# Optimization experiments

Hardware: AMD Instinct MI355X
Metric: run time of the kernel (lower is better)

The kernel has to match this reference:

```python
import jax, jax.numpy as jnp
import numpy as np

K = 3       # kernel_size
STRIDE = 1
PAD = 1
EPS = 1e-12  # F.normalize eps


def setup_inputs() -> dict:
    key = jax.random.key(0)
    k1, k2, k3 = jax.random.split(key, 3)
    x = jax.random.normal(k1, (8, 128, 112, 112), dtype=jnp.float32)
    weight = jax.random.normal(k2, (256, 128, K, K), dtype=jnp.float32)
    bias = jax.random.normal(k3, (256,), dtype=jnp.float32)
    return {"x": x, "weight": weight, "bias": bias}


def reference(x, weight, bias):
    B, C, H, W = x.shape
    Cout = weight.shape[0]
    oh = (H + 2 * PAD - K) // STRIDE + 1
    ow = (W + 2 * PAD - K) // STRIDE + 1
    # im2col: [B, C*K*K, oh, ow]; feature order (C, kh, kw), same as torch F.unfold
    patches = jax.lax.conv_general_dilated_patches(
        x, (K, K), (STRIDE, STRIDE), [(PAD, PAD), (PAD, PAD)],
        dimension_numbers=("NCHW", "OIHW", "NCHW"))
    u = patches.reshape(B, C * K * K, oh * ow)
    # L2-normalize each patch column (dim=1), matching F.normalize(p=2, dim=1)
    norm = jnp.sqrt(jnp.sum(u * u, axis=1, keepdims=True))
    u = u / jnp.maximum(norm, EPS)
    # GEMM: [Cout, C*K*K] x [B, C*K*K, L] -> [B, Cout, L]
    out = jnp.einsum("od,bdl->bol", weight.reshape(Cout, -1), u)
    out = out.reshape(B, Cout, oh, ow) + bias[None, :, None, None]
    return out
```

## Files before the change

kernel.cpp:

```cpp
#include <hip/hip_runtime.h>

#define CIN    128
#define COUT   256
#define Hh     112
#define Ww     112
#define HW     12544
#define NBATCH 8
#define NPIX   (NBATCH*HW)
#define KD     (CIN*9)
#define PH     114
#define PPIX   (NBATCH*PH*PH)

typedef __bf16         v8bf __attribute__((ext_vector_type(8)));
typedef float          v4f  __attribute__((ext_vector_type(4)));

__device__ __forceinline__ unsigned short f2bf(float f) {
  unsigned int u = __float_as_uint(f);
  u += 0x7FFFu + ((u >> 16) & 1u);
  return (unsigned short)(u >> 16);
}

__device__ __forceinline__ void gl_lds16(const void* g, void* l) {
  __builtin_amdgcn_global_load_lds(
      (const __attribute__((address_space(1))) void*)g,
      (__attribute__((address_space(3))) void*)l, 16, 0, 0);
}

#define SQS 65
__global__ __launch_bounds__(256) void k_sq_convert(
    const float* __restrict__ x, unsigned short* __restrict__ xbp,
    float* __restrict__ sq)
{
  __shared__ unsigned int US[56 * SQS];
  __shared__ float sqp[56 * 4];

  int tid = threadIdx.x;
  int l   = tid & 63;
  int wid = tid >> 6;
  int bid = blockIdx.x;
  int xh  = bid & 1;
  int t2  = bid >> 1;
  int b   = t2 / Hh;
  int oy  = t2 - b * Hh;
  int ox0 = xh * 56;

  const float* xp = x + (size_t)b * CIN * HW + oy * Ww + ox0;
  bool valid = l < 56;
  float acc = 0.0f;
#pragma unroll
  for (int it = 0; it < 16; ++it) {
    int cp = it * 4 + wid;
    int c0 = cp * 2;
    float v0 = 0.0f, v1 = 0.0f;
    if (valid) {
      v0 = xp[(size_t)c0 * HW + l];
      v1 = xp[(size_t)(c0 + 1) * HW + l];
    }
    acc += v0 * v0 + v1 * v1;
    unsigned int pk = (unsigned int)f2bf(v0) | ((unsigned int)f2bf(v1) << 16);
    if (valid) US[l * SQS + cp] = pk;
  }
  if (valid) sqp[l * 4 + wid] = acc;
  __syncthreads();

  if (tid < 56) {
    float s = sqp[tid * 4] + sqp[tid * 4 + 1] + sqp[tid * 4 + 2] + sqp[tid * 4 + 3];
    sq[(size_t)b * HW + oy * Ww + ox0 + tid] = s;
  }

  unsigned int* dst = (unsigned int*)xbp +
      ((size_t)(b * PH + oy + 1) * PH + (ox0 + 1)) * (CIN / 2);
  for (int h = tid; h < 896; h += 256) {
    int u0  = h * 4;
    int pix = u0 >> 6, cu = u0 & 63;
    const unsigned int* s = &US[pix * SQS + cu];
    uint4 vv; vv.x = s[0]; vv.y = s[1]; vv.z = s[2]; vv.w = s[3];
    *(uint4*)(dst + u0) = vv;
  }
}

__global__ __launch_bounds__(256) void k_zero_border(unsigned short* __restrict__ xbp)
{
  int gid = blockIdx.x * 256 + threadIdx.x;
  if (gid >= PPIX) return;
  int b  = gid / (PH * PH);
  int r  = gid - b * PH * PH;
  int py = r / PH;
  int px = r - py * PH;
  if (py != 0 && py != PH - 1 && px != 0 && px != PH - 1) return;
  unsigned int* dst = (unsigned int*)xbp + (size_t)gid * (CIN / 2);
  uint4 z = {0, 0, 0, 0};
#pragma unroll
  for (int c0 = 0; c0 < 64; c0 += 4) *(uint4*)(dst + c0) = z;
}

__global__ __launch_bounds__(256) void k_invnorm(
    const float* __restrict__ sq, float* __restrict__ invn)
{
  int p = blockIdx.x * 256 + threadIdx.x;
  if (p >= NPIX) return;
  int b  = p / HW;  int r  = p - b * HW;
  int oy = r / Ww;  int ox = r - oy * Ww;
  const float* s = sq + (size_t)b * HW;
  float acc = 0.0f;
#pragma unroll
  for (int dy = -1; dy <= 1; ++dy) {
    int iy = oy + dy;
    if (iy < 0 || iy >= Hh) continue;
#pragma unroll
    for (int dx = -1; dx <= 1; ++dx) {
      int ix = ox + dx;
      if (ix < 0 || ix >= Ww) continue;
      acc += s[iy * Ww + ix];
    }
  }
  invn[p] = 1.0f / fmaxf(sqrtf(acc), 1e-12f);
}

__global__ __launch_bounds__(256) void k_packw(
    const float* __restrict__ w, unsigned short* __restrict__ wp)
{
  int idx = blockIdx.x * 256 + threadIdx.x;
  int o  = idx / KD;
  int rr = idx - o * KD;
  int kk = rr >> 7;
  int c  = rr & 127;
  wp[idx] = f2bf(w[(size_t)o * KD + c * 9 + kk]);
}

#define SLAB_S 132
__global__ __launch_bounds__(256, 3) void k_conv(
    const unsigned short* __restrict__ wp,
    const unsigned short* __restrict__ xbp,
    const float* __restrict__ invn,
    const float* __restrict__ bias,
    float* __restrict__ out)
{
  __shared__ __align__(16) char smem[64 * SLAB_S * 4];
  unsigned short* As = (unsigned short*)smem;
  unsigned short* Bs = As + 128 * 64;
  float* slab = (float*)smem;

  int tid  = threadIdx.x;
  int lane = tid & 63;
  int wid  = tid >> 6;
  int wm   = wid >> 1, wn = wid & 1;
  int quad = lane >> 4;
  int l16  = lane & 15;

  int L  = blockIdx.x;
  int g  = L >> 4;
  int j  = L & 15;
  int bn = g * 8 + (j & 7);
  int bm = j >> 3;

  int srow = tid >> 3;
  int g16  = (tid & 7) ^ (srow & 7);

  const unsigned short* asrc = wp + (size_t)(bm * 128 + srow) * KD + g16 * 8;

  int pb[4];
#pragma unroll
  for (int jj = 0; jj < 4; ++jj) {
    int n  = bn * 128 + jj * 32 + srow;
    int b  = n / HW;  int r  = n - b * HW;
    int oy = r / Ww;  int ox = r - oy * Ww;
    pb[jj] = ((b * PH + oy) * PH + ox) * CIN + g16 * 8;
  }

  v4f acc[4][4];
#pragma unroll
  for (int mt = 0; mt < 4; ++mt)
#pragma unroll
    for (int nt = 0; nt < 4; ++nt)
#pragma unroll
      for (int q = 0; q < 4; ++q) acc[mt][nt][q] = 0.0f;

  const int khs[9] = {0,0,0,1,1,1,2,2,2};
  const int kws[9] = {0,1,2,0,1,2,0,1,2};

  for (int s = 0; s < 18; ++s) {
    int kk   = s >> 1;
    int c0   = (s & 1) * 64;
    int soff = (khs[kk] * PH + kws[kk]) * CIN + c0;

#pragma unroll
    for (int jj = 0; jj < 4; ++jj)
      gl_lds16(asrc + (size_t)jj * 32 * KD + s * 64,
               &As[(wid * 8 + jj * 32) * 64]);
#pragma unroll
    for (int jj = 0; jj < 4; ++jj)
      gl_lds16(xbp + pb[jj] + soff,
               &Bs[(wid * 8 + jj * 32) * 64]);

    __syncthreads();

#pragma unroll
    for (int h = 0; h < 2; ++h) {
      v8bf af[4], bf[4];
      int cch = (h * 4 + quad) ^ (l16 & 7);
#pragma unroll
      for (int mt = 0; mt < 4; ++mt)
        af[mt] = *(const v8bf*)&As[(wm * 64 + mt * 16 + l16) * 64 + cch * 8];
#pragma unroll
      for (int nt = 0; nt < 4; ++nt)
        bf[nt] = *(const v8bf*)&Bs[(wn * 64 + nt * 16 + l16) * 64 + cch * 8];
#pragma unroll
      for (int mt = 0; mt < 4; ++mt)
#pragma unroll
        for (int nt = 0; nt < 4; ++nt)
          acc[mt][nt] = __builtin_amdgcn_mfma_f32_16x16x32_bf16(
              af[mt], bf[nt], acc[mt][nt], 0, 0, 0);
    }

    __syncthreads();
  }

  int nbase = bn * 128;
  int bb = nbase / HW;
  int rr = nbase - bb * HW;
  float* obase = out + (size_t)bb * COUT * HW + rr;

  float invv[4];
#pragma unroll
  for (int nt = 0; nt < 4; ++nt)
    invv[nt] = invn[nbase + wn * 64 + nt * 16 + l16];

  for (int pass = 0; pass < 2; ++pass) {
    if (pass) __syncthreads();
    if (wm == pass) {
#pragma unroll
      for (int mt = 0; mt < 4; ++mt)
#pragma unroll
        for (int nt = 0; nt < 4; ++nt) {
          int col = wn * 64 + nt * 16 + l16;
#pragma unroll
          for (int reg = 0; reg < 4; ++reg)
            slab[(mt * 16 + quad * 4 + reg) * SLAB_S + col] =
                acc[mt][nt][reg] * invv[nt];
        }
    }
    __syncthreads();
#pragma unroll
    for (int it = 0; it < 2; ++it) {
      int row = it * 32 + (tid >> 3);
      int o   = bm * 128 + pass * 64 + row;
      float bv = bias[o];
      float* orow = obase + (size_t)o * HW;
#pragma unroll
      for (int k = 0; k < 4; ++k) {
        int c4 = ((tid & 7) + k * 8) * 4;
        v4f v = *(const v4f*)&slab[row * SLAB_S + c4];
        v4f r2;
#pragma unroll
        for (int q = 0; q < 4; ++q) r2[q] = v[q] + bv;
        *(v4f*)(orow + c4) = r2;
      }
    }
  }
}

extern "C" void kernel_launch(void* const* d_in, const int* in_sizes, int n_in,
                              void* d_out, int out_size, void* d_ws, size_t ws_size,
                              hipStream_t stream) {
  const float* x    = (const float*)d_in[0];
  const float* w    = (const float*)d_in[1];
  const float* bias = (const float*)d_in[2];
  float* out        = (float*)d_out;

  char* ws = (char*)d_ws;
  unsigned short* xbp = (unsigned short*)ws;
  size_t off = (size_t)PPIX * CIN * 2;
  unsigned short* wpk = (unsigned short*)(ws + off);
  off += (size_t)COUT * KD * 2;
  float* sq = (float*)(ws + off);
  off += (size_t)NPIX * 4;
  float* invn = (float*)(ws + off);

  k_sq_convert<<<NBATCH * Hh * 2, 256, 0, stream>>>(x, xbp, sq);
  k_zero_border<<<(PPIX + 255) / 256, 256, 0, stream>>>(xbp);
  k_packw<<<(COUT * KD) / 256, 256, 0, stream>>>(w, wpk);
  k_invnorm<<<NPIX / 256, 256, 0, stream>>>(sq, invn);
  k_conv<<<1568, 256, 0, stream>>>(wpk, xbp, invn, bias, out);
}
```

Measured before the change: 216.2 us.

## Merge prep kernels into one launch and fold norm stencil into conv epilogue

The four preprocessing kernels (bf16 conversion with squared sums, border zeroing, weight packing, inverse-norm) collapse into a single k_prep launch. Block-index ranges split that launch into conversion, border-only zeroing and vectorized weight-pack work. The 3x3 inverse-norm stencil now runs in the conv epilogue straight from the squared sums. This removes three launches and one intermediate buffer pass, at the cost of extra scattered loads and a division in each conv block's epilogue.

Measured after the change: 218.2 us. About the same (+0.9%).

```diff
diff --git a/kernel.cpp b/kernel.cpp
--- a/kernel.cpp
+++ b/kernel.cpp
@@ -11,6 +11,10 @@
 #define PH     114
 #define PPIX   (NBATCH*PH*PH)
 
+#define G_SQ   784
+#define G_BORD 226
+#define G_PACK 288
+
 typedef __bf16         v8bf __attribute__((ext_vector_type(8)));
 typedef float          v4f  __attribute__((ext_vector_type(4)));
 
@@ -26,113 +30,93 @@
       (__attribute__((address_space(3))) void*)l, 16, 0, 0);
 }
 
-#define SQS 65
-__global__ __launch_bounds__(256) void k_sq_convert(
-    const float* __restrict__ x, unsigned short* __restrict__ xbp,
-    float* __restrict__ sq)
+#define USS 65
+__global__ __launch_bounds__(256) void k_prep(
+    const float* __restrict__ x, const float* __restrict__ w,
+    unsigned short* __restrict__ xbp, float* __restrict__ sq,
+    unsigned short* __restrict__ wp)
 {
-  __shared__ unsigned int US[56 * SQS];
-  __shared__ float sqp[56 * 4];
-
+  int bid = blockIdx.x;
   int tid = threadIdx.x;
-  int l   = tid & 63;
-  int wid = tid >> 6;
-  int bid = blockIdx.x;
-  int xh  = bid & 1;
-  int t2  = bid >> 1;
-  int b   = t2 / Hh;
-  int oy  = t2 - b * Hh;
-  int ox0 = xh * 56;
-
-  const float* xp = x + (size_t)b * CIN * HW + oy * Ww + ox0;
-  bool valid = l < 56;
-  float acc = 0.0f;
-#pragma unroll
-  for (int it = 0; it < 16; ++it) {
-    int cp = it * 4 + wid;
-    int c0 = cp * 2;
-    float v0 = 0.0f, v1 = 0.0f;
-    if (valid) {
-      v0 = xp[(size_t)c0 * HW + l];
-      v1 = xp[(size_t)(c0 + 1) * HW + l];
-    }
-    acc += v0 * v0 + v1 * v1;
-    unsigned int pk = (unsigned int)f2bf(v0) | ((unsigned int)f2bf(v1) << 16);
-    if (valid) US[l * SQS + cp] = pk;
-  }
-  if (valid) sqp[l * 4 + wid] = acc;
-  __syncthreads();
-
-  if (tid < 56) {
-    float s = sqp[tid * 4] + sqp[tid * 4 + 1] + sqp[tid * 4 + 2] + sqp[tid * 4 + 3];
-    sq[(size_t)b * HW + oy * Ww + ox0 + tid] = s;
-  }
-
-  unsigned int* dst = (unsigned int*)xbp +
-      ((size_t)(b * PH + oy + 1) * PH + (ox0 + 1)) * (CIN / 2);
-  for (int h = tid; h < 896; h += 256) {
-    int u0  = h * 4;
-    int pix = u0 >> 6, cu = u0 & 63;
-    const unsigned int* s = &US[pix * SQS + cu];
-    uint4 vv; vv.x = s[0]; vv.y = s[1]; vv.z = s[2]; vv.w = s[3];
-    *(uint4*)(dst + u0) = vv;
-  }
-}
-
-__global__ __launch_bounds__(256) void k_zero_border(unsigned short* __restrict__ xbp)
-{
-  int gid = blockIdx.x * 256 + threadIdx.x;
-  if (gid >= PPIX) return;
-  int b  = gid / (PH * PH);
-  int r  = gid - b * PH * PH;
-  int py = r / PH;
-  int px = r - py * PH;
-  if (py != 0 && py != PH - 1 && px != 0 && px != PH - 1) return;
-  unsigned int* dst = (unsigned int*)xbp + (size_t)gid * (CIN / 2);
-  uint4 z = {0, 0, 0, 0};
-#pragma unroll
-  for (int c0 = 0; c0 < 64; c0 += 4) *(uint4*)(dst + c0) = z;
-}
-
-__global__ __launch_bounds__(256) void k_invnorm(
-    const float* __restrict__ sq, float* __restrict__ invn)
-{
-  int p = blockIdx.x * 256 + threadIdx.x;
-  if (p >= NPIX) return;
-  int b  = p / HW;  int r  = p - b * HW;
-  int oy = r / Ww;  int ox = r - oy * Ww;
-  const float* s = sq + (size_t)b * HW;
-  float acc = 0.0f;
-#pragma unroll
-  for (int dy = -1; dy <= 1; ++dy) {
-    int iy = oy + dy;
-    if (iy < 0 || iy >= Hh) continue;
-#pragma unroll
-    for (int dx = -1; dx <= 1; ++dx) {
-      int ix = ox + dx;
-      if (ix < 0 || ix >= Ww) continue;
-      acc += s[iy * Ww + ix];
-    }
-  }
-  invn[p] = 1.0f / fmaxf(sqrtf(acc), 1e-12f);
-}
-
-__global__ __launch_bounds__(256) void k_packw(
-    const float* __restrict__ w, unsigned short* __restrict__ wp)
-{
-  int idx = blockIdx.x * 256 + threadIdx.x;
-  int o  = idx / KD;
-  int rr = idx - o * KD;
-  int kk = rr >> 7;
-  int c  = rr & 127;
-  wp[idx] = f2bf(w[(size_t)o * KD + c * 9 + kk]);
+
+  if (bid < G_SQ) {
+    __shared__ unsigned int US[128 * USS];
+    __shared__ float sqp[4 * 128];
+
+    int l   = tid & 63;
+    int wid = tid >> 6;
+    int P0  = bid * 128;
+    int b   = P0 / HW;
+    int r0  = P0 - b * HW;
+
+    const float* xb0 = x + (size_t)b * CIN * HW + r0;
+    float ax = 0.0f, ay = 0.0f;
+#pragma unroll
+    for (int i = 0; i < 16; ++i) {
+      int c = wid * 32 + i * 2;
+      float2 v0 = ((const float2*)(xb0 + (size_t)c * HW))[l];
+      float2 v1 = ((const float2*)(xb0 + (size_t)(c + 1) * HW))[l];
+      ax += v0.x * v0.x + v1.x * v1.x;
+      ay += v0.y * v0.y + v1.y * v1.y;
+      int c2 = wid * 16 + i;
+      US[(2 * l) * USS + c2]     = (unsigned int)f2bf(v0.x) | ((unsigned int)f2bf(v1.x) << 16);
+      US[(2 * l + 1) * USS + c2] = (unsigned int)f2bf(v0.y) | ((unsigned int)f2bf(v1.y) << 16);
+    }
+    sqp[wid * 128 + 2 * l]     = ax;
+    sqp[wid * 128 + 2 * l + 1] = ay;
+    __syncthreads();
+
+    if (tid < 128)
+      sq[P0 + tid] = sqp[tid] + sqp[128 + tid] + sqp[256 + tid] + sqp[384 + tid];
+
+    unsigned int* xout = (unsigned int*)xbp;
+#pragma unroll
+    for (int it = 0; it < 8; ++it) {
+      int h  = it * 256 + tid;
+      int px = h >> 4, cu = (h & 15) * 4;
+      const unsigned int* s = &US[px * USS + cu];
+      uint4 v; v.x = s[0]; v.y = s[1]; v.z = s[2]; v.w = s[3];
+      int p  = P0 + px;
+      int rr = p - b * HW;
+      int oy = rr / Ww, ox = rr - oy * Ww;
+      *(uint4*)(xout + ((size_t)(b * PH + oy + 1) * PH + (ox + 1)) * 64 + cu) = v;
+    }
+    return;
+  }
+
+  if (bid < G_SQ + G_BORD) {
+    int h   = (bid - G_SQ) * 256 + tid;
+    int img = h / (452 * 16);
+    int rem = h - img * (452 * 16);
+    int bp  = rem >> 4;
+    int cu  = (rem & 15) * 4;
+    int y, xq;
+    if      (bp < 114) { y = 0;        xq = bp; }
+    else if (bp < 228) { y = PH - 1;   xq = bp - 114; }
+    else if (bp < 340) { y = bp - 227; xq = 0; }
+    else               { y = bp - 339; xq = PH - 1; }
+    uint4 z = {0, 0, 0, 0};
+    *(uint4*)((unsigned int*)xbp + ((size_t)(img * PH + y) * PH + xq) * 64 + cu) = z;
+    return;
+  }
+
+  int idx = (bid - G_SQ - G_BORD) * 256 + tid;
+  int o   = idx / 288;
+  int rem = idx - o * 288;
+  int kk  = rem >> 5;
+  int c0  = (rem & 31) * 4;
+  const float* ws = w + (size_t)o * KD + kk;
+  unsigned int p0 = (unsigned int)f2bf(ws[(c0 + 0) * 9]) | ((unsigned int)f2bf(ws[(c0 + 1) * 9]) << 16);
+  unsigned int p1 = (unsigned int)f2bf(ws[(c0 + 2) * 9]) | ((unsigned int)f2bf(ws[(c0 + 3) * 9]) << 16);
+  uint2 pk; pk.x = p0; pk.y = p1;
+  *(uint2*)((unsigned int*)wp + ((size_t)o * KD + kk * 128 + c0) / 2) = pk;
 }
 
 #define SLAB_S 132
 __global__ __launch_bounds__(256, 3) void k_conv(
     const unsigned short* __restrict__ wp,
     const unsigned short* __restrict__ xbp,
-    const float* __restrict__ invn,
+    const float* __restrict__ sq,
     const float* __restrict__ bias,
     float* __restrict__ out)
 {
@@ -220,11 +204,28 @@
   int bb = nbase / HW;
   int rr = nbase - bb * HW;
   float* obase = out + (size_t)bb * COUT * HW + rr;
+  const float* sqb = sq + (size_t)bb * HW;
 
   float invv[4];
 #pragma unroll
-  for (int nt = 0; nt < 4; ++nt)
-    invv[nt] = invn[nbase + wn * 64 + nt * 16 + l16];
+  for (int nt = 0; nt < 4; ++nt) {
+    int off = wn * 64 + nt * 16 + l16;
+    int rr2 = rr + off;
+    int oy = rr2 / Ww, ox = rr2 - oy * Ww;
+    float ssum = 0.0f;
+#pragma unroll
+    for (int dy = -1; dy <= 1; ++dy) {
+      int iy = oy + dy;
+      if ((unsigned)iy >= (unsigned)Hh) continue;
+#pragma unroll
+      for (int dx = -1; dx <= 1; ++dx) {
+        int ix = ox + dx;
+        if ((unsigned)ix >= (unsigned)Ww) continue;
+        ssum += sqb[iy * Ww + ix];
+      }
+    }
+    invv[nt] = 1.0f / fmaxf(sqrtf(ssum), 1e-12f);
+  }
 
   for (int pass = 0; pass < 2; ++pass) {
     if (pass) __syncthreads();
@@ -274,12 +275,7 @@
   unsigned short* wpk = (unsigned short*)(ws + off);
   off += (size_t)COUT * KD * 2;
   float* sq = (float*)(ws + off);
-  off += (size_t)NPIX * 4;
-  float* invn = (float*)(ws + off);
-
-  k_sq_convert<<<NBATCH * Hh * 2, 256, 0, stream>>>(x, xbp, sq);
-  k_zero_border<<<(PPIX + 255) / 256, 256, 0, stream>>>(xbp);
-  k_packw<<<(COUT * KD) / 256, 256, 0, stream>>>(w, wpk);
-  k_invnorm<<<NPIX / 256, 256, 0, stream>>>(sq, invn);
-  k_conv<<<1568, 256, 0, stream>>>(wpk, xbp, invn, bias, out);
-}
+
+  k_prep<<<G_SQ + G_BORD + G_PACK, 256, 0, stream>>>(x, w, xbp, sq, wpk);
+  k_conv<<<1568, 256, 0, stream>>>(wpk, xbp, sq, bias, out);
+}
```
